# Kernel optimization log

Hardware: AMD Instinct MI355X
Metric: run time of the kernel (lower is better)

## Reference

```python
import jax, jax.numpy as jnp
import numpy as np

WINDOW = 7
EPS = 1e-8


def setup_inputs() -> dict:
    key = jax.random.key(0)
    k1, k2, k3 = jax.random.split(key, 3)
    x = jax.random.normal(k1, (8, 256, 64, 64), dtype=jnp.float32)
    # 1x1 conv weights (bias=False): [out_ch, in_ch]
    w_reduce = jax.random.normal(k2, (64, 256), dtype=jnp.float32) * 0.05
    w_proj = jax.random.normal(k3, (512, 64), dtype=jnp.float32) * 0.1
    return {"x": x, "w_reduce": w_reduce, "w_proj": w_proj}


def _unfold_window(feat, window):
    # feat: [b, c, h, w] -> patches: [b, c, window*window, h, w]
    b, c, h, w = feat.shape
    pad = window // 2
    fp = jnp.pad(feat, ((0, 0), (0, 0), (pad, pad), (pad, pad)))
    # fixed small loop over window^2 = 49 shifts (matches F.unfold ordering)
    return jnp.stack(
        [fp[:, :, i:i + h, j:j + w] for i in range(window) for j in range(window)],
        axis=2,
    )


def reference(x, w_reduce, w_proj):
    window = WINDOW
    # reduce: 1x1 conv, no bias
    feat = jnp.einsum('oc,bchw->bohw', w_reduce, x)  # [b, cr, h, w]
    patches = _unfold_window(feat, window)           # [b, cr, K, h, w], K=49
    # cosine similarity between center feature and each window patch (dim=channel)
    dot = jnp.einsum('bchw,bckhw->bkhw', feat, patches)          # [b, K, h, w]
    cn = jnp.sqrt(jnp.sum(feat * feat, axis=1))                  # [b, h, w]
    pn = jnp.sqrt(jnp.sum(patches * patches, axis=1))            # [b, K, h, w]
    sim = dot / jnp.maximum(cn[:, None] * pn, EPS)               # [b, K, h, w]
    att = jax.nn.softmax(sim, axis=1)                            # softmax over window dim
    corr = jnp.einsum('bkhw,bckhw->bchw', att, patches)          # [b, cr, h, w]
    # proj: 1x1 conv, no bias
    return jnp.einsum('oc,bchw->bohw', w_proj, corr)             # [b, out, h, w]
```

## Files before the change

### kernel.cpp

```cpp
#include <hip/hip_runtime.h>
#include <stdint.h>

#define NPIX 4096
#define CIN  256
#define CR   64
#define COUT 512
#define NB   8
#define CG   256
#define FT   128

typedef _Float16 half8 __attribute__((ext_vector_type(8)));
typedef _Float16 half4 __attribute__((ext_vector_type(4)));
typedef _Float16 half2v __attribute__((ext_vector_type(2)));
typedef float f32x4 __attribute__((ext_vector_type(4)));

__device__ __forceinline__ float dpp8_sum(float d) {
  int y;
  y = __builtin_amdgcn_update_dpp(0, __float_as_int(d), 0xB1, 0xF, 0xF, true);
  d += __int_as_float(y);
  y = __builtin_amdgcn_update_dpp(0, __float_as_int(d), 0x4E, 0xF, 0xF, true);
  d += __int_as_float(y);
  y = __builtin_amdgcn_update_dpp(0, __float_as_int(d), 0x141, 0xF, 0xF, true);
  d += __int_as_float(y);
  return d;
}

__global__ __launch_bounds__(256) void k0_prep(
    const float* __restrict__ wr, const float* __restrict__ wp,
    _Float16* __restrict__ wrAh, _Float16* __restrict__ wrAl,
    _Float16* __restrict__ wpH,
    float* __restrict__ cnormG, float* __restrict__ featTail)
{
  const int tid = blockIdx.x * 256 + threadIdx.x;
  if (tid < 16384) {
    const int j = tid & 7, l = (tid >> 3) & 63;
    const int kt = (tid >> 9) & 7, mt = tid >> 12;
    const int m = mt * 16 + (l & 15);
    const int k = kt * 32 + (l >> 4) * 8 + j;
    const float v = wr[m * CIN + k];
    const _Float16 h = (_Float16)v;
    wrAh[tid] = h;
    wrAl[tid] = (_Float16)(v - (float)h);
  } else if (tid < 16384 + COUT * CR) {
    const int fi = tid - 16384;
    const int j = fi & 7, l = (fi >> 3) & 63;
    const int kt = (fi >> 9) & 1, ot = (fi >> 10) & 3, g = fi >> 12;
    const int o = g * 64 + ot * 16 + (l & 15);
    const int k = kt * 32 + (l >> 4) * 8 + j;
    wpH[fi] = (_Float16)wp[o * CR + k];
  } else {
    const int gi = tid - (16384 + COUT * CR);
    if (gi < CG)               cnormG[gi] = 0.f;
    else if (gi < 2 * CG)      cnormG[CG + NB * NPIX + (gi - CG)] = 0.f;
    else if (gi < 2 * CG + FT) featTail[gi - 2 * CG] = 0.f;
  }
}

__global__ __launch_bounds__(512) void k1_reduce(
    const float* __restrict__ x,
    const _Float16* __restrict__ wrAh, const _Float16* __restrict__ wrAl,
    _Float16* __restrict__ feat_h, float* __restrict__ cnorm)
{
  const int blk = blockIdx.x;
  const int b = blk >> 6, seg = blk & 63;
  const int t = threadIdx.x, lane = t & 63;
  const int g = __builtin_amdgcn_readfirstlane((int)t >> 6);
  const int nt = g & 3, mth = g >> 2;
  const int col = lane & 15, krow = lane >> 4;

  const float* xb = x + (size_t)b * CIN * NPIX + seg * 64 + nt * 16 + col;

  f32x4 c0 = {0.f, 0.f, 0.f, 0.f};
  f32x4 c1 = {0.f, 0.f, 0.f, 0.f};

#pragma unroll
  for (int kt = 0; kt < 8; ++kt) {
    half8 Bh, Bl;
    const float* xk = xb + (size_t)(kt * 32 + krow * 8) * NPIX;
#pragma unroll
    for (int j = 0; j < 8; ++j) {
      const float v = xk[(size_t)j * NPIX];
      const _Float16 h = (_Float16)v;
      Bh[j] = h;
      Bl[j] = (_Float16)(v - (float)h);
    }
    const int fi0 = ((mth * 2 + 0) * 8 + kt) * 512 + lane * 8;
    const int fi1 = ((mth * 2 + 1) * 8 + kt) * 512 + lane * 8;
    const half8 Ah0 = *(const half8*)(wrAh + fi0);
    const half8 Al0 = *(const half8*)(wrAl + fi0);
    const half8 Ah1 = *(const half8*)(wrAh + fi1);
    const half8 Al1 = *(const half8*)(wrAl + fi1);
    c0 = __builtin_amdgcn_mfma_f32_16x16x32_f16(Ah0, Bh, c0, 0, 0, 0);
    c0 = __builtin_amdgcn_mfma_f32_16x16x32_f16(Ah0, Bl, c0, 0, 0, 0);
    c0 = __builtin_amdgcn_mfma_f32_16x16x32_f16(Al0, Bh, c0, 0, 0, 0);
    c1 = __builtin_amdgcn_mfma_f32_16x16x32_f16(Ah1, Bh, c1, 0, 0, 0);
    c1 = __builtin_amdgcn_mfma_f32_16x16x32_f16(Ah1, Bl, c1, 0, 0, 0);
    c1 = __builtin_amdgcn_mfma_f32_16x16x32_f16(Al1, Bh, c1, 0, 0, 0);
  }

  const int px = seg * 64 + nt * 16 + col;
  _Float16* fb = feat_h + ((size_t)b * NPIX + px) * 64;
  const int ch0 = mth * 32 + krow * 4;
  half4 v0, v1;
  float p = 0.f;
#pragma unroll
  for (int r = 0; r < 4; ++r) {
    v0[r] = (_Float16)c0[r];
    v1[r] = (_Float16)c1[r];
    p = fmaf(c0[r], c0[r], p);
    p = fmaf(c1[r], c1[r], p);
  }
  *(half4*)(fb + ch0) = v0;
  *(half4*)(fb + ch0 + 16) = v1;

  p += __shfl_xor(p, 16);
  p += __shfl_xor(p, 32);

  __shared__ float cn[8][16];
  if (lane < 16) cn[g][lane] = p;
  __syncthreads();
  if (t < 64) {
    const int nt2 = t >> 4, c16 = t & 15;
    cnorm[b * NPIX + seg * 64 + t] = sqrtf(cn[nt2][c16] + cn[nt2 + 4][c16]);
  }
}

__global__ __launch_bounds__(512, 4) void k23_fused(
    const _Float16* __restrict__ feat_h, const float* __restrict__ cnorm,
    const _Float16* __restrict__ wpH, float* __restrict__ out)
{
  const int blk = blockIdx.x;
  const int b = blk & 7, h = blk >> 3;
  const int t = threadIdx.x;
  const int lane = t & 63;
  const int g = __builtin_amdgcn_readfirstlane((int)t >> 6);
  const int w = t >> 3;
  const int cb = (t & 7) * 8;
  const int px = h * 64 + w;
  const int gpx = b * NPIX + px;

  const float* cnb = cnorm + b * NPIX;

  __shared__ __align__(16) _Float16 fs[2][72][72];
  __shared__ float cnS[2][80];
  __shared__ __align__(16) _Float16 corrH[4096];

  half8 rS0, rS1;
  float rc = 0.f;

  auto LOAD = [&](int ar) {
    const long rowb = ((long)b * NPIX + ar * 64 - 4) * 64;
    rS0 = *(const half8*)(feat_h + rowb + (long)t * 8);
    if (t < 64) rS1 = *(const half8*)(feat_h + rowb + (long)(512 + t) * 8);
    if (t < 72) rc = cnb[ar * 64 - 4 + t];
  };
  auto WRITE = [&](int bufi) {
    *(half8*)&fs[bufi][t >> 3][(t & 7) * 8] = rS0;
    if (t < 64) *(half8*)&fs[bufi][64 + (t >> 3)][(t & 7) * 8] = rS1;
    if (t < 72) cnS[bufi][t] = rc;
  };

  half2v fc2[4];
  {
    const half8 fcv = *(const half8*)(feat_h + ((size_t)b * NPIX + px) * 64 + cb);
#pragma unroll
    for (int i = 0; i < 4; ++i) { fc2[i][0] = fcv[2*i]; fc2[i][1] = fcv[2*i+1]; }
  }
  const float cnc = cnorm[gpx];

  half2v accA[4], accB[4];
#pragma unroll
  for (int i = 0; i < 4; ++i) {
    accA[i] = (half2v)(_Float16)0.f;
    accB[i] = (half2v)(_Float16)0.f;
  }

  const int lo = (h - 3 < 0) ? 0 : h - 3;
  const int hi = (h + 3 > 63) ? 63 : h + 3;
  float l = 7.0f * (float)(6 - (hi - lo));

  LOAD(lo);
  WRITE(0);
  __syncthreads();

  int buf = 0;
  for (int ar = lo; ar <= hi; ++ar) {
    if (ar < hi) LOAD(ar + 1);
#pragma unroll
    for (int dx = -3; dx <= 3; ++dx) {
      const int j = w + 4 + dx;
      const half8 nv = *(const half8*)&fs[buf][j][cb];
      half2v n0, n1, n2, n3;
      n0[0] = nv[0]; n0[1] = nv[1];
      n1[0] = nv[2]; n1[1] = nv[3];
      n2[0] = nv[4]; n2[1] = nv[5];
      n3[0] = nv[6]; n3[1] = nv[7];
      float d = 0.f;
      d = __builtin_amdgcn_fdot2(fc2[0], n0, d, false);
      d = __builtin_amdgcn_fdot2(fc2[1], n1, d, false);
      d = __builtin_amdgcn_fdot2(fc2[2], n2, d, false);
      d = __builtin_amdgcn_fdot2(fc2[3], n3, d, false);
      d = dpp8_sum(d);
      const float cnk = cnS[buf][j];
      float sim = d * __builtin_amdgcn_rcpf(fmaxf(cnc * cnk, 1e-8f));
      const bool valid = (unsigned)(w + dx) < 64u;
      sim = valid ? sim : 0.f;
      const float p = __expf(sim);
      l += p;
      const float pv = valid ? p : 0.f;
      const _Float16 ph = (_Float16)pv;
      half2v ph2; ph2[0] = ph; ph2[1] = ph;
      if (dx & 1) {
        accA[0] = ph2 * n0 + accA[0];
        accA[1] = ph2 * n1 + accA[1];
        accA[2] = ph2 * n2 + accA[2];
        accA[3] = ph2 * n3 + accA[3];
      } else {
        accB[0] = ph2 * n0 + accB[0];
        accB[1] = ph2 * n1 + accB[1];
        accB[2] = ph2 * n2 + accB[2];
        accB[3] = ph2 * n3 + accB[3];
      }
    }
    if (ar < hi) WRITE(buf ^ 1);
    __syncthreads();
    buf ^= 1;
  }

  {
    const float inv = __builtin_amdgcn_rcpf(l);
    half8 hv;
#pragma unroll
    for (int i = 0; i < 4; ++i) {
      const float a0 = (float)accA[i][0] + (float)accB[i][0];
      const float a1 = (float)accA[i][1] + (float)accB[i][1];
      hv[2*i]   = (_Float16)(a0 * inv);
      hv[2*i+1] = (_Float16)(a1 * inv);
    }
    const int wbyte = (w * 128 + (cb << 1)) ^ ((w & 7) << 4);
    *(half8*)((char*)corrH + wbyte) = hv;
  }
  __syncthreads();

  const _Float16* wA = wpH + (size_t)g * 4096;
  float* outb = out + ((size_t)b * COUT + g * 64) * NPIX + h * 64;
#pragma unroll
  for (int pt = 0; pt < 4; ++pt) {
    half8 Bf0, Bf1;
    {
      const int pxl = pt * 16 + (lane & 15);
      const int sw = (pxl & 7) << 4;
      const int rowb = pxl * 128 + ((lane >> 4) << 4);
      Bf0 = *(const half8*)((const char*)corrH + (rowb ^ sw));
      Bf1 = *(const half8*)((const char*)corrH + ((rowb + 64) ^ sw));
    }
#pragma unroll
    for (int ot = 0; ot < 4; ++ot) {
      f32x4 c = {0.f, 0.f, 0.f, 0.f};
      const half8 A0 = *(const half8*)(wA + (ot * 2 + 0) * 512 + lane * 8);
      const half8 A1 = *(const half8*)(wA + (ot * 2 + 1) * 512 + lane * 8);
      c = __builtin_amdgcn_mfma_f32_16x16x32_f16(A0, Bf0, c, 0, 0, 0);
      c = __builtin_amdgcn_mfma_f32_16x16x32_f16(A1, Bf1, c, 0, 0, 0);
      float* op = outb + (size_t)(ot * 16 + ((lane >> 4) << 2)) * NPIX
                       + pt * 16 + (lane & 15);
#pragma unroll
      for (int r = 0; r < 4; ++r) op[(size_t)r * NPIX] = c[r];
    }
  }
}

extern "C" void kernel_launch(void* const* d_in, const int* in_sizes, int n_in,
                              void* d_out, int out_size, void* d_ws, size_t ws_size,
                              hipStream_t stream)
{
  const float* x  = (const float*)d_in[0];
  const float* wr = (const float*)d_in[1];
  const float* wp = (const float*)d_in[2];
  float* out = (float*)d_out;

  float* ws = (float*)d_ws;
  _Float16* wrAh  = (_Float16*)ws;
  _Float16* wrAl  = (_Float16*)(ws + 8192);
  _Float16* wpH   = (_Float16*)(ws + 16384);
  float* cnormG   = ws + 32768;
  float* cnorm    = cnormG + CG;
  _Float16* feat_h = (_Float16*)(cnorm + NB * NPIX + CG);
  float* featTail = (float*)(feat_h + (size_t)NB * NPIX * 64);

  hipLaunchKernelGGL(k0_prep,   dim3(195), dim3(256), 0, stream, wr, wp, wrAh, wrAl, wpH, cnormG, featTail);
  hipLaunchKernelGGL(k1_reduce, dim3(512), dim3(512), 0, stream, x, wrAh, wrAl, feat_h, cnorm);
  hipLaunchKernelGGL(k23_fused, dim3(512), dim3(512), 0, stream, feat_h, cnorm, wpH, out);
}
```

Baseline: 41.10 us.

## Drop weight-prep kernel; convert weights in-kernel and precompute inverse norms

Removes the separate preparation kernel by having the reduce kernel read fp32 w_reduce directly and split it into hi/lo fp16 fragments in registers. The fused kernel now loads w_proj fp32 and converts it to fp16 MFMA fragments before the barrier. The halo zeroing moves into block 0 of the reduce kernel. Norms are stored as clamped reciprocal square roots, so the similarity becomes two multiplies instead of a reciprocal. This saves one launch and its serialization, at the cost of redundant weight loads and conversions in every block, plus a slightly different epsilon clamp semantics.

Result: slower. 48.12 us (+17.1%).

```diff
diff --git a/kernel.cpp b/kernel.cpp
--- a/kernel.cpp
+++ b/kernel.cpp
@@ -6,8 +6,6 @@
 #define CR   64
 #define COUT 512
 #define NB   8
-#define CG   256
-#define FT   128
 
 typedef _Float16 half8 __attribute__((ext_vector_type(8)));
 typedef _Float16 half4 __attribute__((ext_vector_type(4)));
@@ -25,41 +23,20 @@
   return d;
 }
 
-__global__ __launch_bounds__(256) void k0_prep(
-    const float* __restrict__ wr, const float* __restrict__ wp,
-    _Float16* __restrict__ wrAh, _Float16* __restrict__ wrAl,
-    _Float16* __restrict__ wpH,
-    float* __restrict__ cnormG, float* __restrict__ featTail)
-{
-  const int tid = blockIdx.x * 256 + threadIdx.x;
-  if (tid < 16384) {
-    const int j = tid & 7, l = (tid >> 3) & 63;
-    const int kt = (tid >> 9) & 7, mt = tid >> 12;
-    const int m = mt * 16 + (l & 15);
-    const int k = kt * 32 + (l >> 4) * 8 + j;
-    const float v = wr[m * CIN + k];
-    const _Float16 h = (_Float16)v;
-    wrAh[tid] = h;
-    wrAl[tid] = (_Float16)(v - (float)h);
-  } else if (tid < 16384 + COUT * CR) {
-    const int fi = tid - 16384;
-    const int j = fi & 7, l = (fi >> 3) & 63;
-    const int kt = (fi >> 9) & 1, ot = (fi >> 10) & 3, g = fi >> 12;
-    const int o = g * 64 + ot * 16 + (l & 15);
-    const int k = kt * 32 + (l >> 4) * 8 + j;
-    wpH[fi] = (_Float16)wp[o * CR + k];
-  } else {
-    const int gi = tid - (16384 + COUT * CR);
-    if (gi < CG)               cnormG[gi] = 0.f;
-    else if (gi < 2 * CG)      cnormG[CG + NB * NPIX + (gi - CG)] = 0.f;
-    else if (gi < 2 * CG + FT) featTail[gi - 2 * CG] = 0.f;
+__device__ __forceinline__ void hilo8(const float4 a, const float4 b,
+                                      half8& h, half8& l) {
+  const float v[8] = {a.x, a.y, a.z, a.w, b.x, b.y, b.z, b.w};
+#pragma unroll
+  for (int j = 0; j < 8; ++j) {
+    const _Float16 hh = (_Float16)v[j];
+    h[j] = hh;
+    l[j] = (_Float16)(v[j] - (float)hh);
   }
 }
 
 __global__ __launch_bounds__(512) void k1_reduce(
-    const float* __restrict__ x,
-    const _Float16* __restrict__ wrAh, const _Float16* __restrict__ wrAl,
-    _Float16* __restrict__ feat_h, float* __restrict__ cnorm)
+    const float* __restrict__ x, const float* __restrict__ wr,
+    _Float16* __restrict__ feat_h, float* __restrict__ icn)
 {
   const int blk = blockIdx.x;
   const int b = blk >> 6, seg = blk & 63;
@@ -68,7 +45,18 @@
   const int nt = g & 3, mth = g >> 2;
   const int col = lane & 15, krow = lane >> 4;
 
+  if (blk == 0) {
+    if (t < 8) icn[(int)t - 8] = 0.f;
+    if (t >= 8 && t < 80) icn[NB * NPIX + (int)t - 8] = 0.f;
+    float* fgh = (float*)feat_h;
+    if (t < 256) fgh[(int)t - 256] = 0.f;
+    float* fgt = (float*)feat_h + (size_t)NB * NPIX * 32;
+    if (t < 256) fgt[t] = 0.f;
+  }
+
   const float* xb = x + (size_t)b * CIN * NPIX + seg * 64 + nt * 16 + col;
+  const float* wrm0 = wr + (size_t)((mth * 2 + 0) * 16 + col) * CIN + krow * 8;
+  const float* wrm1 = wr + (size_t)((mth * 2 + 1) * 16 + col) * CIN + krow * 8;
 
   f32x4 c0 = {0.f, 0.f, 0.f, 0.f};
   f32x4 c1 = {0.f, 0.f, 0.f, 0.f};
@@ -84,12 +72,11 @@
       Bh[j] = h;
       Bl[j] = (_Float16)(v - (float)h);
     }
-    const int fi0 = ((mth * 2 + 0) * 8 + kt) * 512 + lane * 8;
-    const int fi1 = ((mth * 2 + 1) * 8 + kt) * 512 + lane * 8;
-    const half8 Ah0 = *(const half8*)(wrAh + fi0);
-    const half8 Al0 = *(const half8*)(wrAl + fi0);
-    const half8 Ah1 = *(const half8*)(wrAh + fi1);
-    const half8 Al1 = *(const half8*)(wrAl + fi1);
+    half8 Ah0, Al0, Ah1, Al1;
+    hilo8(*(const float4*)(wrm0 + kt * 32), *(const float4*)(wrm0 + kt * 32 + 4),
+          Ah0, Al0);
+    hilo8(*(const float4*)(wrm1 + kt * 32), *(const float4*)(wrm1 + kt * 32 + 4),
+          Ah1, Al1);
     c0 = __builtin_amdgcn_mfma_f32_16x16x32_f16(Ah0, Bh, c0, 0, 0, 0);
     c0 = __builtin_amdgcn_mfma_f32_16x16x32_f16(Ah0, Bl, c0, 0, 0, 0);
     c0 = __builtin_amdgcn_mfma_f32_16x16x32_f16(Al0, Bh, c0, 0, 0, 0);
@@ -121,13 +108,14 @@
   __syncthreads();
   if (t < 64) {
     const int nt2 = t >> 4, c16 = t & 15;
-    cnorm[b * NPIX + seg * 64 + t] = sqrtf(cn[nt2][c16] + cn[nt2 + 4][c16]);
+    const float ss = cn[nt2][c16] + cn[nt2 + 4][c16];
+    icn[b * NPIX + seg * 64 + t] = rsqrtf(fmaxf(ss, 1e-16f));
   }
 }
 
 __global__ __launch_bounds__(512, 4) void k23_fused(
-    const _Float16* __restrict__ feat_h, const float* __restrict__ cnorm,
-    const _Float16* __restrict__ wpH, float* __restrict__ out)
+    const _Float16* __restrict__ feat_h, const float* __restrict__ icn,
+    const float* __restrict__ wp, float* __restrict__ out)
 {
   const int blk = blockIdx.x;
   const int b = blk & 7, h = blk >> 3;
@@ -139,7 +127,7 @@
   const int px = h * 64 + w;
   const int gpx = b * NPIX + px;
 
-  const float* cnb = cnorm + b * NPIX;
+  const float* cnb = icn + b * NPIX;
 
   __shared__ __align__(16) _Float16 fs[2][72][72];
   __shared__ float cnS[2][80];
@@ -166,7 +154,7 @@
 #pragma unroll
     for (int i = 0; i < 4; ++i) { fc2[i][0] = fcv[2*i]; fc2[i][1] = fcv[2*i+1]; }
   }
-  const float cnc = cnorm[gpx];
+  const float icnc = icn[gpx];
 
   half2v accA[4], accB[4];
 #pragma unroll
@@ -201,8 +189,8 @@
       d = __builtin_amdgcn_fdot2(fc2[2], n2, d, false);
       d = __builtin_amdgcn_fdot2(fc2[3], n3, d, false);
       d = dpp8_sum(d);
-      const float cnk = cnS[buf][j];
-      float sim = d * __builtin_amdgcn_rcpf(fmaxf(cnc * cnk, 1e-8f));
+      const float icnk = cnS[buf][j];
+      float sim = d * icnc * icnk;
       const bool valid = (unsigned)(w + dx) < 64u;
       sim = valid ? sim : 0.f;
       const float p = __expf(sim);
@@ -240,9 +228,25 @@
     const int wbyte = (w * 128 + (cb << 1)) ^ ((w & 7) << 4);
     *(half8*)((char*)corrH + wbyte) = hv;
   }
+
+  half8 Af[8];
+#pragma unroll
+  for (int ot = 0; ot < 4; ++ot)
+#pragma unroll
+    for (int k2 = 0; k2 < 2; ++k2) {
+      const float* wpp = wp + (size_t)(g * 64 + ot * 16 + (lane & 15)) * 64
+                       + k2 * 32 + (lane >> 4) * 8;
+      const float4 lo4 = *(const float4*)wpp;
+      const float4 hi4 = *(const float4*)(wpp + 4);
+      half8 a;
+      a[0] = (_Float16)lo4.x; a[1] = (_Float16)lo4.y;
+      a[2] = (_Float16)lo4.z; a[3] = (_Float16)lo4.w;
+      a[4] = (_Float16)hi4.x; a[5] = (_Float16)hi4.y;
+      a[6] = (_Float16)hi4.z; a[7] = (_Float16)hi4.w;
+      Af[ot * 2 + k2] = a;
+    }
   __syncthreads();
 
-  const _Float16* wA = wpH + (size_t)g * 4096;
   float* outb = out + ((size_t)b * COUT + g * 64) * NPIX + h * 64;
 #pragma unroll
   for (int pt = 0; pt < 4; ++pt) {
@@ -257,10 +261,8 @@
 #pragma unroll
     for (int ot = 0; ot < 4; ++ot) {
       f32x4 c = {0.f, 0.f, 0.f, 0.f};
-      const half8 A0 = *(const half8*)(wA + (ot * 2 + 0) * 512 + lane * 8);
-      const half8 A1 = *(const half8*)(wA + (ot * 2 + 1) * 512 + lane * 8);
-      c = __builtin_amdgcn_mfma_f32_16x16x32_f16(A0, Bf0, c, 0, 0, 0);
-      c = __builtin_amdgcn_mfma_f32_16x16x32_f16(A1, Bf1, c, 0, 0, 0);
+      c = __builtin_amdgcn_mfma_f32_16x16x32_f16(Af[ot * 2 + 0], Bf0, c, 0, 0, 0);
+      c = __builtin_amdgcn_mfma_f32_16x16x32_f16(Af[ot * 2 + 1], Bf1, c, 0, 0, 0);
       float* op = outb + (size_t)(ot * 16 + ((lane >> 4) << 2)) * NPIX
                        + pt * 16 + (lane & 15);
 #pragma unroll
@@ -279,15 +281,9 @@
   float* out = (float*)d_out;
 
   float* ws = (float*)d_ws;
-  _Float16* wrAh  = (_Float16*)ws;
-  _Float16* wrAl  = (_Float16*)(ws + 8192);
-  _Float16* wpH   = (_Float16*)(ws + 16384);
-  float* cnormG   = ws + 32768;
-  float* cnorm    = cnormG + CG;
-  _Float16* feat_h = (_Float16*)(cnorm + NB * NPIX + CG);
-  float* featTail = (float*)(feat_h + (size_t)NB * NPIX * 64);
-
-  hipLaunchKernelGGL(k0_prep,   dim3(195), dim3(256), 0, stream, wr, wp, wrAh, wrAl, wpH, cnormG, featTail);
-  hipLaunchKernelGGL(k1_reduce, dim3(512), dim3(512), 0, stream, x, wrAh, wrAl, feat_h, cnorm);
-  hipLaunchKernelGGL(k23_fused, dim3(512), dim3(512), 0, stream, feat_h, cnorm, wpH, out);
-}
+  float* icn = ws + 8;
+  _Float16* feat_h = (_Float16*)(ws + 8 + NB * NPIX + 72 + 256);
+
+  hipLaunchKernelGGL(k1_reduce, dim3(512), dim3(512), 0, stream, x, wr, feat_h, icn);
+  hipLaunchKernelGGL(k23_fused, dim3(512), dim3(512), 0, stream, feat_h, icn, wp, out);
+}
```
